# Kernel tuning notes

Hardware: AMD Instinct MI355X
Metric: run time of the kernel (lower is better)

## Reference

```python
import jax, jax.numpy as jnp
import numpy as np

B, C, D, H, W = 2, 2, 64, 256, 256
EPS = 1e-6
ALPHA = 5.0
TTEMP = 0.7


def _grids():
    gy, gx = jnp.meshgrid(jnp.arange(H, dtype=jnp.float32),
                          jnp.arange(W, dtype=jnp.float32), indexing='ij')
    return gy, gx


def _extract_targets(centerlines, gy, gx):
    # centerlines: [B,1,D,H,W] int labels {0,1,2}. For each (b,d) slice: if label i
    # occurs exactly once, target = (y,x) of that pixel, else negpair (-1,-1).
    cl = centerlines[:, 0]  # [B,D,H,W]
    out = []
    for lbl in (1, 2):
        m = (cl == lbl).astype(jnp.float32)
        cnt = m.sum(axis=(-2, -1))            # [B,D]
        ys = (m * gy).sum(axis=(-2, -1))
        xs = (m * gx).sum(axis=(-2, -1))
        t = jnp.where((cnt == 1.0)[..., None], jnp.stack([ys, xs], axis=-1), -1.0)
        out.append(t)                          # [B,D,2] float32
    return out


def _d2(gy, gx, target):
    # torch PairwiseDistance adds eps to the difference: ||x1-x2+eps||_2
    # -> [B,1,D,H,W]
    dy = gy[None, None, None] - target[:, None, :, 0, None, None] + EPS
    dx = gx[None, None, None] - target[:, None, :, 1, None, None] + EPS
    return jnp.sqrt(dy * dy + dx * dx)


def total_loss(logits, centerlines, radiuses):
    probs = jax.nn.sigmoid(logits)             # [B,2,D,H,W]
    gy, gx = _grids()
    targets = _extract_targets(centerlines, gy, gx)
    d2s = [_d2(gy, gx, t) for t in targets]
    # art masks: relu(exp(d2/r1 - 1) - 1) then filled with 1 where >0  ==  (d2 > r1);
    # the in-place fill makes it gradient-free, so treat as constant {0,1} mask.
    arts = [jax.lax.stop_gradient((d2s[k] > radiuses[k, 1]).astype(jnp.float32))
            for k in range(2)]
    arts = [arts[1], arts[0]]                  # swapped, exactly as in the source
    valid = [(t[:, :, 0] != -1.0).astype(jnp.float32) for t in targets]  # [B,D]

    # ---- CenterDistanceLoss ----
    loss_cent = jnp.float32(0.0)
    for k in range(2):
        art = arts[k]                                            # [B,1,D,H,W]
        denom = (probs * art).sum(axis=(1, 3, 4)) + EPS          # [B,D]
        y_cnt = (art * gy * probs).sum(axis=(1, 3, 4)) / denom
        x_cnt = (art * gx * probs).sum(axis=(1, 3, 4)) / denom
        cnt = jnp.stack([y_cnt, x_cnt], axis=-1)                 # [B,D,2]
        diff = cnt - targets[k] + EPS
        l2 = jnp.sqrt((diff * diff).sum(-1)) * valid[k]
        loss_cent = loss_cent + l2.mean()

    # ---- RadiusConstraintLoss ----
    loss_cnst = jnp.float32(0.0)
    for k in range(2):
        r_lu, r_ow = radiuses[k, 0], radiuses[k, 1]
        vm = valid[k][:, None, :, None, None]                    # [B,1,D,1,1]
        d2 = d2s[k]
        art = arts[k]
        lu_dout = jax.nn.relu(1.0 - jnp.exp(1.0 - d2 / r_lu)) / ALPHA * vm * art
        ow_dout = jax.nn.relu(1.0 - jnp.exp(1.0 - d2 / r_ow)) / ALPHA * vm * art
        p_lu, p_ow = probs[:, :1], probs[:, 1:]
        rc_out = ((lu_dout * p_lu).sum(axis=(1, 3, 4)) / (p_lu.sum(axis=(1, 3, 4)) + EPS)
                  + (ow_dout * p_ow).sum(axis=(1, 3, 4)) / (p_ow.sum(axis=(1, 3, 4)) + EPS))
        lu_din = jax.nn.relu(jnp.exp(1.0 - d2 / r_lu) - 1.0) * vm
        ow_din = jax.nn.relu(jnp.exp(1.0 - d2 / r_ow) - 1.0) * vm
        rc_in = ((lu_din * (1.0 - p_lu)).sum(axis=(1, 3, 4)) / (r_lu * r_lu * jnp.pi)
                 + (ow_din * (1.0 - p_ow)).sum(axis=(1, 3, 4)) / (r_ow * r_ow * jnp.pi))
        loss_cnst = loss_cnst + rc_out.mean() + rc_in.mean()

    # ---- ConsistencyLoss ----  (F.softmax default dim=1 for 5-D; BCE clamps log >= -100)
    p_orig = jax.lax.stop_gradient(jax.nn.softmax(logits[:, :, 1:-1] / TTEMP, axis=1))
    p_shift = jax.nn.softmax(logits[:, :, 0:-2] / TTEMP, axis=1)
    log_p = jnp.maximum(jnp.log(p_orig), -100.0)
    log_1mp = jnp.maximum(jnp.log(1.0 - p_orig), -100.0)
    loss_csis = -(p_shift * log_p + (1.0 - p_shift) * log_1mp).mean()

    return 0.02 * loss_cent + 1.0 * loss_cnst + 0.001 * loss_csis


def setup_inputs():
    key = jax.random.key(0)
    k1, k2, k3, k4, k5 = jax.random.split(key, 5)
    logits = jax.random.normal(k1, (B, C, D, H, W), dtype=jnp.float32)
    # place exactly one ICA(=1) and one ECA(=2) marker per (b,d) slice
    ys1 = jax.random.randint(k2, (B * D,), 0, H)
    xs1 = jax.random.randint(k3, (B * D,), 0, W)
    ys2 = jax.random.randint(k4, (B * D,), 0, H)
    xs2 = jax.random.randint(k5, (B * D,), 0, W)
    bi = jnp.repeat(jnp.arange(B), D)
    di = jnp.tile(jnp.arange(D), B)
    cl = jnp.zeros((B, 1, D, H, W), dtype=jnp.int32)
    cl = cl.at[bi, 0, di, ys1, xs1].set(1)
    cl = cl.at[bi, 0, di, ys2, xs2].set(2)
    cl = cl.at[:, :, 0].set(0)  # exercise the negpair (-1,-1) path
    radiuses = jnp.array([[4.0, 7.0], [5.0, 8.0]], dtype=jnp.float32)
    return {"logits": logits, "centerlines": cl, "radiuses": radiuses}


def reference(logits, centerlines, radiuses):
    return total_loss(logits, centerlines, radiuses)
```

## Files before the change

### kernel.cpp

```cpp
#include <hip/hip_runtime.h>
#include <math.h>

#define BB 2
#define CC 2
#define DD 64
#define HW 65536
#define NROW 128
#define EPSF 1e-6f
#define ALPHAF 5.0f
#define LOG2E 1.44269504089f
#define LN2 0.69314718056f
#define INV_T (1.0f/0.7f)
#define C_SH (INV_T*LOG2E)

struct Ws {
  float tgt[2][NROW][2];
  float valid[2][NROW];
  float part[NROW][2][17];
};

struct RowCtx {
  float t0y, t0x, t1y, t1x;
  float r01sq, r11sq;
  float c00, c01, c10, c11;
};

template<bool N0, bool N1>
__device__ __forceinline__ void do_row(const float4& v0, const float4& v1,
                                       const float4& w0, const float4& w1,
                                       float yf, float x0f,
                                       const RowCtx& cx, float* acc)
{
  const float a0[4] = {v0.x, v0.y, v0.z, v0.w};
  const float a1[4] = {v1.x, v1.y, v1.z, v1.w};
  const float b0[4] = {w0.x, w0.y, w0.z, w0.w};
  const float b1[4] = {w1.x, w1.y, w1.z, w1.w};
  float rp0 = 0.f, rp1 = 0.f, rcs = 0.f, rpsx = 0.f;
  float rA0 = 0.f, rA0x = 0.f, rT00 = 0.f, rT01 = 0.f;
  float rA1 = 0.f, rA1x = 0.f, rT10 = 0.f, rT11 = 0.f;
  const float dy0 = yf - cx.t0y;
  const float dy0sq = dy0 * dy0;
  const float dy1 = yf - cx.t1y;
  const float dy1sq = dy1 * dy1;
#pragma unroll
  for (int e = 0; e < 4; ++e) {
    const float le0 = a0[e], le1 = a1[e];
    const float p0 = __builtin_amdgcn_rcpf(1.f + __expf(-le0));
    const float p1 = __builtin_amdgcn_rcpf(1.f + __expf(-le1));
    rp0 += p0; rp1 += p1;
    const float psum = p0 + p1;
    const float gxf = x0f + (float)e;

    const float dshn = (le1 - le0) * C_SH;
    const float psig = __builtin_amdgcn_rcpf(1.f + exp2f(dshn));
    const float dor2 = (b0[e] - b1[e]) * C_SH;
    const float lg  = log2f(1.f + exp2f(-fabsf(dor2)));
    const float sp2 = fmaxf(dor2, 0.f) + lg;
    rcs += psig * dor2 - sp2;

    float ap0 = p0, ap1 = p1, bp0 = p0, bp1 = p1;
    float d0sq = 0.f, d1sq = 0.f;
    if (N1) {
      const float dx1 = gxf - cx.t1x;
      d1sq = fmaf(dx1, dx1, dy1sq);
      const float art0 = (d1sq > cx.r11sq) ? 1.f : 0.f;
      ap0 = art0 * p0; ap1 = art0 * p1;
      const float a0p = ap0 + ap1;
      rA0 += a0p; rA0x = fmaf(gxf, a0p, rA0x);
      if (!N0) { rT00 += ap0; rT01 += ap1; }
    }
    if (N0) {
      const float dx0 = gxf - cx.t0x;
      d0sq = fmaf(dx0, dx0, dy0sq);
      const float art1 = (d0sq > cx.r01sq) ? 1.f : 0.f;
      bp0 = art1 * p0; bp1 = art1 * p1;
      const float a1p = bp0 + bp1;
      rA1 += a1p; rA1x = fmaf(gxf, a1p, rA1x);
      if (!N1) { rT10 += bp0; rT11 += bp1; }
    }
    if (!N0 || !N1) rpsx = fmaf(gxf, psum, rpsx);

    if (N0) {
      const float dist0 = __builtin_amdgcn_sqrtf(d0sq);
      const float elu0 = exp2f(fmaf(dist0, -cx.c00, LOG2E));
      const float eow0 = exp2f(fmaf(dist0, -cx.c01, LOG2E));
      acc[8]  = fmaf(fmaxf(1.f - elu0, 0.f), ap0, acc[8]);
      acc[9]  = fmaf(fmaxf(1.f - eow0, 0.f), ap1, acc[9]);
      acc[10] = fmaf(fmaxf(elu0 - 1.f, 0.f), 1.f - p0, acc[10]);
      acc[11] = fmaf(fmaxf(eow0 - 1.f, 0.f), 1.f - p1, acc[11]);
    }
    if (N1) {
      const float dist1 = __builtin_amdgcn_sqrtf(d1sq);
      const float elu1 = exp2f(fmaf(dist1, -cx.c10, LOG2E));
      const float eow1 = exp2f(fmaf(dist1, -cx.c11, LOG2E));
      acc[12] = fmaf(fmaxf(1.f - elu1, 0.f), bp0, acc[12]);
      acc[13] = fmaf(fmaxf(1.f - eow1, 0.f), bp1, acc[13]);
      acc[14] = fmaf(fmaxf(elu1 - 1.f, 0.f), 1.f - p0, acc[14]);
      acc[15] = fmaf(fmaxf(eow1 - 1.f, 0.f), 1.f - p1, acc[15]);
    }
  }
  acc[6] += rp0; acc[7] += rp1; acc[16] += rcs;
  const float rps = rp0 + rp1;
  if (N1) { acc[0] += rA0; acc[1] = fmaf(yf, rA0, acc[1]); acc[2] += rA0x; }
  else    { acc[0] += rps; acc[1] = fmaf(yf, rps, acc[1]); acc[2] += rpsx; }
  if (N0) { acc[3] += rA1; acc[4] = fmaf(yf, rA1, acc[4]); acc[5] += rA1x; }
  else    { acc[3] += rps; acc[4] = fmaf(yf, rps, acc[4]); acc[5] += rpsx; }
  if (!N0) { acc[8]  += N1 ? rT00 : rp0; acc[9]  += N1 ? rT01 : rp1; }
  if (!N1) { acc[12] += N0 ? rT10 : rp0; acc[13] += N0 ? rT11 : rp1; }
}

#define DISPATCH_ROW(V0,V1,W0,W1,YF)                                       \
  { const bool nr0 = fabsf((YF) - cx.t0y) <= cut0;                         \
    const bool nr1 = fabsf((YF) - cx.t1y) <= cut1;                         \
    if (nr0) { if (nr1) do_row<true ,true >(V0,V1,W0,W1,YF,x0f,cx,acc);    \
               else     do_row<true ,false>(V0,V1,W0,W1,YF,x0f,cx,acc); }  \
    else     { if (nr1) do_row<false,true >(V0,V1,W0,W1,YF,x0f,cx,acc);    \
               else     do_row<false,false>(V0,V1,W0,W1,YF,x0f,cx,acc); } }

__global__ __launch_bounds__(1024) void k_all(const float* __restrict__ logits,
                                              const int* __restrict__ cl,
                                              const float* __restrict__ rad,
                                              Ws* __restrict__ ws)
{
  const int xcd  = blockIdx.x & 7;
  const int slot = blockIdx.x >> 3;
  const int row  = xcd * 16 + (slot >> 1);
  const int half = slot & 1;
  const int tid  = threadIdx.x;
  const int lane = tid & 63;
  const int wid  = tid >> 6;
  const int b = row >> 6, d = row & 63;

  __shared__ int sacc[6];
  if (tid < 6) sacc[tid] = 0;
  __syncthreads();
  {
    const int4* cp = (const int4*)(cl + ((long long)row << 16));
#pragma unroll 8
    for (int j = 0; j < 16; ++j) {
      const int idx4 = tid + (j << 10);
      const int4 v = cp[idx4];
      if ((v.x | v.y | v.z | v.w) != 0) {
        const int vv[4] = {v.x, v.y, v.z, v.w};
#pragma unroll
        for (int e = 0; e < 4; ++e) {
          const int val = vv[e];
          if (val == 1 || val == 2) {
            const int hw = (idx4 << 2) + e;
            const int k3 = (val - 1) * 3;
            atomicAdd(&sacc[k3 + 0], 1);
            atomicAdd(&sacc[k3 + 1], hw >> 8);
            atomicAdd(&sacc[k3 + 2], hw & 255);
          }
        }
      }
    }
  }
  __syncthreads();
  const int c0 = sacc[0], c1 = sacc[3];
  const float t0y = (c0 == 1) ? (float)sacc[1] : -1.f;
  const float t0x = (c0 == 1) ? (float)sacc[2] : -1.f;
  const float t1y = (c1 == 1) ? (float)sacc[4] : -1.f;
  const float t1x = (c1 == 1) ? (float)sacc[5] : -1.f;
  if (half == 0 && tid == 0) {
    ws->tgt[0][row][0] = t0y; ws->tgt[0][row][1] = t0x;
    ws->valid[0][row] = (c0 == 1) ? 1.f : 0.f;
    ws->tgt[1][row][0] = t1y; ws->tgt[1][row][1] = t1x;
    ws->valid[1][row] = (c1 == 1) ? 1.f : 0.f;
  }

  const float r00 = rad[0], r01 = rad[1], r10 = rad[2], r11 = rad[3];
  RowCtx cx;
  cx.t0y = t0y - EPSF; cx.t0x = t0x - EPSF;
  cx.t1y = t1y - EPSF; cx.t1x = t1x - EPSF;
  cx.r01sq = r01 * r01; cx.r11sq = r11 * r11;
  cx.c00 = LOG2E / r00; cx.c01 = LOG2E / r01;
  cx.c10 = LOG2E / r10; cx.c11 = LOG2E / r11;
  const float cut0 = 6.f * r01, cut1 = 6.f * r11;

  const float* l0 = logits + (((long long)(b * CC + 0) * DD + d) << 16);
  const float* l1 = logits + (((long long)(b * CC + 1) * DD + d) << 16);
  const bool do_csis = (d < DD - 2);
  const long long noff = do_csis ? HW : 0;
  const float* m0 = l0 + noff;
  const float* m1 = l1 + noff;

  float acc[17];
#pragma unroll
  for (int i = 0; i < 17; ++i) acc[i] = 0.f;

  const float x0f = (float)(lane << 2);
  int y = half + (wid << 1);
  int p = (y << 8) + (lane << 2);

  float4 v0 = *(const float4*)(l0 + p);
  float4 v1 = *(const float4*)(l1 + p);
  float4 w0 = *(const float4*)(m0 + p);
  float4 w1 = *(const float4*)(m1 + p);

#pragma unroll 1
  for (int j = 0; j < 7; ++j) {
    const int pn = p + 32 * 256;
    float4 nv0 = *(const float4*)(l0 + pn);
    float4 nv1 = *(const float4*)(l1 + pn);
    float4 nw0 = *(const float4*)(m0 + pn);
    float4 nw1 = *(const float4*)(m1 + pn);
    const float yf = (float)y;
    DISPATCH_ROW(v0, v1, w0, w1, yf);
    v0 = nv0; v1 = nv1; w0 = nw0; w1 = nw1; p = pn; y += 32;
  }
  { const float yf = (float)y;
    DISPATCH_ROW(v0, v1, w0, w1, yf); }

  __shared__ float pl[16][17];
#pragma unroll
  for (int i = 0; i < 17; ++i) {
    float v = acc[i];
#pragma unroll
    for (int off = 32; off > 0; off >>= 1) v += __shfl_down(v, off, 64);
    if (lane == 0) pl[wid][i] = v;
  }
  __syncthreads();
  if (tid < 17) {
    float s = 0.f;
#pragma unroll
    for (int w = 0; w < 16; ++w) s += pl[w][tid];
    if (tid == 16) s *= (do_csis ? LN2 : 0.f);
    ws->part[row][half][tid] = s;
  }
}

__global__ void k_final(const float* __restrict__ rad,
                        const Ws* __restrict__ ws, float* __restrict__ out) {
  __shared__ float red[3][NROW];
  const int r = threadIdx.x;
  const float PI = 3.14159265358979323846f;
  float cent = 0.0f, cnst = 0.0f, csis = 0.0f;
  if (r < NROW) {
    float s[17];
#pragma unroll
    for (int i = 0; i < 17; ++i)
      s[i] = ws->part[r][0][i] + ws->part[r][1][i];

    const float P0 = s[6], P1 = s[7];
#pragma unroll
    for (int k = 0; k < 2; ++k) {
      const float vld = ws->valid[k][r];
      const float denom = s[3 * k + 0] + EPSF;
      const float yc = s[3 * k + 1] / denom;
      const float xc = s[3 * k + 2] / denom;
      const float dy = yc - ws->tgt[k][r][0] + EPSF;
      const float dx = xc - ws->tgt[k][r][1] + EPSF;
      cent += sqrtf(dy * dy + dx * dx) * vld;
      const float r_lu = rad[2 * k], r_ow = rad[2 * k + 1];
      const int o = 8 + 4 * k;
      const float rc_out = (s[o]     / (ALPHAF * (P0 + EPSF)) +
                            s[o + 1] / (ALPHAF * (P1 + EPSF))) * vld;
      const float rc_in  = (s[o + 2] / (r_lu * r_lu * PI) +
                            s[o + 3] / (r_ow * r_ow * PI)) * vld;
      cnst += rc_out + rc_in;
    }
    csis = s[16];
  }
  red[0][r] = cent; red[1][r] = cnst; red[2][r] = csis;
  __syncthreads();
  for (int st = NROW / 2; st > 0; st >>= 1) {
    if (r < st) {
      red[0][r] += red[0][r + st];
      red[1][r] += red[1][r + st];
      red[2][r] += red[2][r + st];
    }
    __syncthreads();
  }
  if (r == 0) {
    const float inv_rows = 1.0f / (float)NROW;
    const float loss_cent = red[0][0] * inv_rows;
    const float loss_cnst = red[1][0] * inv_rows;
    const float loss_csis = -red[2][0] / (float)((long long)BB * (DD - 2) * HW);
    out[0] = 0.02f * loss_cent + loss_cnst + 0.001f * loss_csis;
  }
}

extern "C" void kernel_launch(void* const* d_in, const int* in_sizes, int n_in,
                              void* d_out, int out_size, void* d_ws, size_t ws_size,
                              hipStream_t stream) {
  const float* logits = (const float*)d_in[0];
  const int*   cl     = (const int*)d_in[1];
  const float* rad    = (const float*)d_in[2];
  Ws* ws = (Ws*)d_ws;

  k_all<<<2 * NROW, 1024, 0, stream>>>(logits, cl, rad, ws);
  k_final<<<1, NROW, 0, stream>>>(rad, ws, (float*)d_out);
}
```

Before: 37.74 us.

## Share exp/log between shifted sigmoid and softplus terms; prefetch logits before target scan

Splits the CSIS loss into a product term and a softplus term. Each pixel now reuses one exp2/log2/rcp of the current slice's logit difference for both the sigmoid and the log-softplus, and the softplus sum is attributed to the neighbouring slice through the csa/csb masks. This removes one exp2 and one log2 per element. The first logit float4 loads are also moved ahead of the centerline scan and its syncthreads so their latency overlaps the scan. The cost is one extra accumulator and register pressure from the loads held across the scan.

```diff
diff --git a/kernel.cpp b/kernel.cpp
--- a/kernel.cpp
+++ b/kernel.cpp
@@ -35,7 +35,7 @@
   const float a1[4] = {v1.x, v1.y, v1.z, v1.w};
   const float b0[4] = {w0.x, w0.y, w0.z, w0.w};
   const float b1[4] = {w1.x, w1.y, w1.z, w1.w};
-  float rp0 = 0.f, rp1 = 0.f, rcs = 0.f, rpsx = 0.f;
+  float rp0 = 0.f, rp1 = 0.f, rprod = 0.f, rsp = 0.f, rpsx = 0.f;
   float rA0 = 0.f, rA0x = 0.f, rT00 = 0.f, rT01 = 0.f;
   float rA1 = 0.f, rA1x = 0.f, rT10 = 0.f, rT11 = 0.f;
   const float dy0 = yf - cx.t0y;
@@ -51,12 +51,14 @@
     const float psum = p0 + p1;
     const float gxf = x0f + (float)e;
 
-    const float dshn = (le1 - le0) * C_SH;
-    const float psig = __builtin_amdgcn_rcpf(1.f + exp2f(dshn));
-    const float dor2 = (b0[e] - b1[e]) * C_SH;
-    const float lg  = log2f(1.f + exp2f(-fabsf(dor2)));
-    const float sp2 = fmaxf(dor2, 0.f) + lg;
-    rcs += psig * dor2 - sp2;
+    const float t = (le1 - le0) * C_SH;
+    const float E = exp2f(-fabsf(t));
+    const float R = __builtin_amdgcn_rcpf(1.f + E);
+    const float L = log2f(1.f + E);
+    const float psig = (t >= 0.f ? E : 1.f) * R;
+    const float dorn = (b0[e] - b1[e]) * C_SH;
+    rprod = fmaf(psig, dorn, rprod);
+    rsp  += fmaxf(-t, 0.f) + L;
 
     float ap0 = p0, ap1 = p1, bp0 = p0, bp1 = p1;
     float d0sq = 0.f, d1sq = 0.f;
@@ -99,7 +101,7 @@
       acc[15] = fmaf(fmaxf(eow1 - 1.f, 0.f), 1.f - p1, acc[15]);
     }
   }
-  acc[6] += rp0; acc[7] += rp1; acc[16] += rcs;
+  acc[6] += rp0; acc[7] += rp1; acc[16] += rprod; acc[17] += rsp;
   const float rps = rp0 + rp1;
   if (N1) { acc[0] += rA0; acc[1] = fmaf(yf, rA0, acc[1]); acc[2] += rA0x; }
   else    { acc[0] += rps; acc[1] = fmaf(yf, rps, acc[1]); acc[2] += rpsx; }
@@ -131,6 +133,23 @@
   const int wid  = tid >> 6;
   const int b = row >> 6, d = row & 63;
 
+  const float* l0 = logits + (((long long)(b * CC + 0) * DD + d) << 16);
+  const float* l1 = logits + (((long long)(b * CC + 1) * DD + d) << 16);
+  const bool csa = (d < DD - 2);
+  const bool csb = (d >= 1) && (d <= DD - 2);
+  const long long noff = csa ? HW : 0;
+  const float* m0 = l0 + noff;
+  const float* m1 = l1 + noff;
+
+  const float x0f = (float)(lane << 2);
+  int y = half + (wid << 1);
+  int p = (y << 8) + (lane << 2);
+
+  float4 v0 = *(const float4*)(l0 + p);
+  float4 v1 = *(const float4*)(l1 + p);
+  float4 w0 = *(const float4*)(m0 + p);
+  float4 w1 = *(const float4*)(m1 + p);
+
   __shared__ int sacc[6];
   if (tid < 6) sacc[tid] = 0;
   __syncthreads();
@@ -178,25 +197,9 @@
   cx.c10 = LOG2E / r10; cx.c11 = LOG2E / r11;
   const float cut0 = 6.f * r01, cut1 = 6.f * r11;
 
-  const float* l0 = logits + (((long long)(b * CC + 0) * DD + d) << 16);
-  const float* l1 = logits + (((long long)(b * CC + 1) * DD + d) << 16);
-  const bool do_csis = (d < DD - 2);
-  const long long noff = do_csis ? HW : 0;
-  const float* m0 = l0 + noff;
-  const float* m1 = l1 + noff;
-
-  float acc[17];
-#pragma unroll
-  for (int i = 0; i < 17; ++i) acc[i] = 0.f;
-
-  const float x0f = (float)(lane << 2);
-  int y = half + (wid << 1);
-  int p = (y << 8) + (lane << 2);
-
-  float4 v0 = *(const float4*)(l0 + p);
-  float4 v1 = *(const float4*)(l1 + p);
-  float4 w0 = *(const float4*)(m0 + p);
-  float4 w1 = *(const float4*)(m1 + p);
+  float acc[18];
+#pragma unroll
+  for (int i = 0; i < 18; ++i) acc[i] = 0.f;
 
 #pragma unroll 1
   for (int j = 0; j < 7; ++j) {
@@ -212,9 +215,9 @@
   { const float yf = (float)y;
     DISPATCH_ROW(v0, v1, w0, w1, yf); }
 
-  __shared__ float pl[16][17];
-#pragma unroll
-  for (int i = 0; i < 17; ++i) {
+  __shared__ float pl[16][18];
+#pragma unroll
+  for (int i = 0; i < 18; ++i) {
     float v = acc[i];
 #pragma unroll
     for (int off = 32; off > 0; off >>= 1) v += __shfl_down(v, off, 64);
@@ -222,10 +225,17 @@
   }
   __syncthreads();
   if (tid < 17) {
-    float s = 0.f;
-#pragma unroll
-    for (int w = 0; w < 16; ++w) s += pl[w][tid];
-    if (tid == 16) s *= (do_csis ? LN2 : 0.f);
+    float s;
+    if (tid == 16) {
+      float prod = 0.f, sp = 0.f;
+#pragma unroll
+      for (int w = 0; w < 16; ++w) { prod += pl[w][16]; sp += pl[w][17]; }
+      s = (csa ? prod * LN2 : 0.f) - (csb ? sp * LN2 : 0.f);
+    } else {
+      s = 0.f;
+#pragma unroll
+      for (int w = 0; w < 16; ++w) s += pl[w][tid];
+    }
     ws->part[row][half][tid] = s;
   }
 }
```

After: 37.93 us. About the same (+0.5%).
